# Optimization experiments

Hardware: AMD Instinct MI355X
Metric: run time of the kernel (lower is better)

Reference implementation:

```python
import jax, jax.numpy as jnp
import numpy as np

N = 50000      # nodes
E = 800000     # edges (avg degree 16)
D = 256        # d_model
H = 8          # heads
C = D // H     # per-head channels = 32
DE = 64        # edge feature dim
NEG_SLOPE = 0.2
EPS = 1e-5


def setup_inputs() -> dict:
    key = jax.random.key(0)
    ks = jax.random.split(key, 12)
    s = 0.05
    return {
        "x": jax.random.normal(ks[0], (N, D), jnp.float32),
        "edge_attr": jax.random.normal(ks[1], (E, DE), jnp.float32),
        "edge_index": jax.random.randint(ks[2], (2, E), 0, N, dtype=jnp.int32),
        # GATv2Conv params (torch Linear layout: [out, in])
        "W_l": jax.random.normal(ks[3], (H * C, D), jnp.float32) * s,   # lin_l (source)
        "b_l": jnp.zeros((H * C,), jnp.float32),
        "W_r": jax.random.normal(ks[4], (H * C, D), jnp.float32) * s,   # lin_r (target)
        "b_r": jnp.zeros((H * C,), jnp.float32),
        "W_e": jax.random.normal(ks[5], (H * C, DE), jnp.float32) * s,  # lin_edge (no bias)
        "att": jax.random.normal(ks[6], (H, C), jnp.float32) * s,       # attention vector a
        "W_res": jax.random.normal(ks[7], (H * C, D), jnp.float32) * s, # residual Linear (no bias)
        "bias": jnp.zeros((H * C,), jnp.float32),                        # conv output bias
        "gamma": jnp.ones((D,), jnp.float32),                            # LayerNorm weight
        "beta": jnp.zeros((D,), jnp.float32),                            # LayerNorm bias
    }


def reference(x, edge_attr, W_l, b_l, W_r, b_r, W_e, att, W_res, bias, gamma, beta, edge_index):
    src = edge_index[0]  # j (messages flow source -> target)
    dst = edge_index[1]  # i

    xl = (x @ W_l.T + b_l).reshape(N, H, C)   # source transform
    xr = (x @ W_r.T + b_r).reshape(N, H, C)   # target transform
    ee = (edge_attr @ W_e.T).reshape(E, H, C)  # edge embedding

    # GATv2 attention logits per edge/head
    g = jax.nn.leaky_relu(xl[src] + xr[dst] + ee, NEG_SLOPE)  # [E, H, C]
    alpha = jnp.einsum("ehc,hc->eh", g, att)                   # [E, H]

    # segment softmax over incoming edges of each target node
    amax = jax.ops.segment_max(alpha, dst, num_segments=N)     # [N, H] (-inf for empty)
    ealpha = jnp.exp(alpha - amax[dst])
    denom = jax.ops.segment_sum(ealpha, dst, num_segments=N)   # [N, H]
    alpha = ealpha / jnp.where(denom > 0, denom, 1.0)[dst]

    # weighted message aggregation (scatter-add)
    msg = xl[src] * alpha[:, :, None]                          # [E, H, C]
    out = jax.ops.segment_sum(msg, dst, num_segments=N)        # [N, H, C]

    out = out.reshape(N, H * C) + x @ W_res.T + bias           # concat heads + residual + bias

    # LayerNorm over last dim
    mu = out.mean(-1, keepdims=True)
    var = ((out - mu) ** 2).mean(-1, keepdims=True)
    return (out - mu) * jax.lax.rsqrt(var + EPS) * gamma + beta
```

## Files before the change

kernel.cpp:

```cpp
#include <hip/hip_runtime.h>

#define N_NODES 50000
#define N_EDGES 800000
#define D_MODEL 256
#define H_HEADS 8
#define C_CH 32
#define DE_DIM 64
#define NEG_SLOPE 0.2f
#define LN_EPS 1e-5f
#define TILES (N_EDGES / 64)

typedef float  f32x4  __attribute__((ext_vector_type(4)));
typedef short  bf16x8 __attribute__((ext_vector_type(8)));

static __device__ __forceinline__ unsigned short f2bf(float f) {
    unsigned int u = __float_as_uint(f);
    u += 0x7fffu + ((u >> 16) & 1u);
    return (unsigned short)(u >> 16);
}
static __device__ __forceinline__ float bf2f(unsigned short s) {
    return __uint_as_float(((unsigned int)s) << 16);
}
static __device__ __forceinline__ bf16x8 load_cvt8(const float* __restrict__ p) {
    float4 a = *(const float4*)p;
    float4 b = *(const float4*)(p + 4);
    bf16x8 r;
    r[0] = (short)f2bf(a.x); r[1] = (short)f2bf(a.y);
    r[2] = (short)f2bf(a.z); r[3] = (short)f2bf(a.w);
    r[4] = (short)f2bf(b.x); r[5] = (short)f2bf(b.y);
    r[6] = (short)f2bf(b.z); r[7] = (short)f2bf(b.w);
    return r;
}

__global__ __launch_bounds__(256) void cvt_bf16_kernel(const float* __restrict__ in,
                                                       unsigned short* __restrict__ out,
                                                       int n8) {
    int g = blockIdx.x * 256 + threadIdx.x;
    if (g < n8) {
        bf16x8 v = load_cvt8(in + (size_t)g * 8);
        *(bf16x8*)(out + (size_t)g * 8) = v;
    }
}

__global__ __launch_bounds__(256) void node_gemm(const unsigned short* __restrict__ xbf,
                                                 const unsigned short* __restrict__ Wbf,
                                                 const float* __restrict__ bl,
                                                 const float* __restrict__ br,
                                                 unsigned short* __restrict__ xl,
                                                 unsigned short* __restrict__ xr,
                                                 float* __restrict__ res) {
    int tid = threadIdx.x;
    int lane = tid & 63, wv = tid >> 6;
    int quad = lane >> 4, l15 = lane & 15;
    int rowTile = blockIdx.x * 64;
    int which = blockIdx.y;
    const unsigned short* W = Wbf + (size_t)which * 65536;
    int colBase = wv * 64;

    f32x4 acc[4][4];
#pragma unroll
    for (int r = 0; r < 4; r++)
#pragma unroll
        for (int c = 0; c < 4; c++) acc[r][c] = (f32x4){0.f, 0.f, 0.f, 0.f};

#pragma unroll 1
    for (int k8 = 0; k8 < 8; ++k8) {
        int kb = k8 * 32 + quad * 8;
        bf16x8 af[4], bfr[4];
#pragma unroll
        for (int r = 0; r < 4; r++) {
            int row = rowTile + r * 16 + l15;
            if (row > N_NODES - 1) row = N_NODES - 1;
            af[r] = *(const bf16x8*)(xbf + (size_t)row * D_MODEL + kb);
        }
#pragma unroll
        for (int c = 0; c < 4; c++) {
            int col = colBase + c * 16 + l15;
            bfr[c] = *(const bf16x8*)(W + (size_t)col * D_MODEL + kb);
        }
#pragma unroll
        for (int r = 0; r < 4; r++)
#pragma unroll
            for (int c = 0; c < 4; c++)
                acc[r][c] = __builtin_amdgcn_mfma_f32_16x16x32_bf16(af[r], bfr[c], acc[r][c], 0, 0, 0);
    }

    float bv[4];
#pragma unroll
    for (int c = 0; c < 4; c++) {
        int col = colBase + c * 16 + l15;
        bv[c] = (which == 0) ? bl[col] : (which == 1 ? br[col] : 0.f);
    }
#pragma unroll
    for (int r = 0; r < 4; r++) {
#pragma unroll
        for (int g = 0; g < 4; g++) {
            int row = rowTile + r * 16 + quad * 4 + g;
            if (row < N_NODES) {
#pragma unroll
                for (int c = 0; c < 4; c++) {
                    int col = colBase + c * 16 + l15;
                    float v = acc[r][c][g] + bv[c];
                    size_t idx = (size_t)row * D_MODEL + col;
                    if (which == 0)      xl[idx] = f2bf(v);
                    else if (which == 1) xr[idx] = f2bf(v);
                    else                 res[idx] = v;
                }
            }
        }
    }
}

__global__ __launch_bounds__(256) void edge_logits(const float* __restrict__ edge_attr,
                                                   const float* __restrict__ We,
                                                   const float* __restrict__ att,
                                                   const int* __restrict__ srcIdx,
                                                   const int* __restrict__ dstIdx,
                                                   const int* __restrict__ posOf,
                                                   const unsigned short* __restrict__ xl,
                                                   const unsigned short* __restrict__ xr,
                                                   float* __restrict__ alphaP) {
    __shared__ short weS[2048 * 8];

    int tid = threadIdx.x;
    int lane = tid & 63, wv = tid >> 6;
    int quad = lane >> 4, l15 = lane & 15;

    for (int g = tid; g < 2048; g += 256) {
        int c = g >> 7, kq = (g >> 6) & 1, ln = g & 63;
        int o = c * 16 + (ln & 15);
        int k = kq * 32 + (ln >> 4) * 8;
        bf16x8 v = load_cvt8(We + o * DE_DIM + k);
        *(bf16x8*)&weS[g * 8] = v;
    }
    __syncthreads();

    for (int tile = blockIdx.x; tile < TILES; tile += gridDim.x) {
        int e = tile * 64 + wv * 16 + l15;
        int srcv = srcIdx[e];
        int dstv = dstIdx[e];
        int posv = posOf[e];

        bf16x8 a0 = load_cvt8(edge_attr + (size_t)e * DE_DIM + quad * 8);
        bf16x8 a1 = load_cvt8(edge_attr + (size_t)e * DE_DIM + 32 + quad * 8);

        const unsigned short* xlr = xl + (size_t)srcv * D_MODEL + quad * 4;
        const unsigned short* xrr = xr + (size_t)dstv * D_MODEL + quad * 4;

        float pa[8];
#pragma unroll
        for (int h = 0; h < 8; h++) pa[h] = 0.f;

#pragma unroll
        for (int c = 0; c < 16; c++) {
            bf16x8 b0 = *(bf16x8*)&weS[((c * 2 + 0) * 64 + lane) * 8];
            bf16x8 b1 = *(bf16x8*)&weS[((c * 2 + 1) * 64 + lane) * 8];
            f32x4 ee = (f32x4){0.f, 0.f, 0.f, 0.f};
            ee = __builtin_amdgcn_mfma_f32_16x16x32_bf16(b0, a0, ee, 0, 0, 0);
            ee = __builtin_amdgcn_mfma_f32_16x16x32_bf16(b1, a1, ee, 0, 0, 0);
            ushort4 x4 = *(const ushort4*)(xlr + c * 16);
            ushort4 r4 = *(const ushort4*)(xrr + c * 16);
            f32x4 av = *(const f32x4*)(att + c * 16 + quad * 4);
            float s = 0.f;
            float t0 = ee[0] + bf2f(x4.x) + bf2f(r4.x);
            float t1 = ee[1] + bf2f(x4.y) + bf2f(r4.y);
            float t2 = ee[2] + bf2f(x4.z) + bf2f(r4.z);
            float t3 = ee[3] + bf2f(x4.w) + bf2f(r4.w);
            t0 = (t0 > 0.f) ? t0 : NEG_SLOPE * t0;
            t1 = (t1 > 0.f) ? t1 : NEG_SLOPE * t1;
            t2 = (t2 > 0.f) ? t2 : NEG_SLOPE * t2;
            t3 = (t3 > 0.f) ? t3 : NEG_SLOPE * t3;
            s = fmaf(t0, av[0], s);
            s = fmaf(t1, av[1], s);
            s = fmaf(t2, av[2], s);
            s = fmaf(t3, av[3], s);
            pa[c >> 1] += s;
        }
#pragma unroll
        for (int h = 0; h < 8; h++) {
            float v = pa[h];
            v += __shfl_xor(v, 16);
            v += __shfl_xor(v, 32);
            pa[h] = v;
        }
        if (quad == 0) {
            float4 w0 = make_float4(pa[0], pa[1], pa[2], pa[3]);
            *(float4*)(alphaP + (size_t)posv * 8) = w0;
        } else if (quad == 1) {
            float4 w1 = make_float4(pa[4], pa[5], pa[6], pa[7]);
            *(float4*)(alphaP + (size_t)posv * 8 + 4) = w1;
        }
    }
}

__global__ __launch_bounds__(256) void hist_kernel(const int* __restrict__ dstIdx,
                                                   int* __restrict__ cnt) {
    int e = blockIdx.x * 256 + threadIdx.x;
    if (e < N_EDGES) atomicAdd(&cnt[dstIdx[e]], 1);
}

__global__ __launch_bounds__(1024) void scan_kernel(const int* __restrict__ cnt,
                                                    int* __restrict__ off,
                                                    int* __restrict__ woff) {
    const int CHUNK = 49;
    int tid = threadIdx.x;
    int base = tid * CHUNK;
    int local[CHUNK];
    int sum = 0;
#pragma unroll
    for (int j = 0; j < CHUNK; ++j) {
        int idx = base + j;
        int v = (idx < N_NODES) ? cnt[idx] : 0;
        local[j] = sum;
        sum += v;
    }
    int lane = tid & 63, wv = tid >> 6;
    int s = sum;
#pragma unroll
    for (int ofs = 1; ofs < 64; ofs <<= 1) {
        int t2 = __shfl_up(s, ofs);
        if (lane >= ofs) s += t2;
    }
    __shared__ int wsum[16];
    __shared__ int woffS[16];
    if (lane == 63) wsum[wv] = s;
    __syncthreads();
    if (tid == 0) {
        int a = 0;
#pragma unroll
        for (int i = 0; i < 16; ++i) { woffS[i] = a; a += wsum[i]; }
    }
    __syncthreads();
    int excl = woffS[wv] + (s - sum);
#pragma unroll
    for (int j = 0; j < CHUNK; ++j) {
        int idx = base + j;
        if (idx < N_NODES) {
            int v = excl + local[j];
            off[idx] = v;
            woff[idx] = v;
        }
    }
    if (tid == 0) off[N_NODES] = N_EDGES;
}

__global__ __launch_bounds__(256) void scatter_kernel(const int* __restrict__ srcIdx,
                                                      const int* __restrict__ dstIdx,
                                                      int* __restrict__ woff,
                                                      int* __restrict__ posOf,
                                                      int* __restrict__ srcP) {
    int e = blockIdx.x * 256 + threadIdx.x;
    if (e < N_EDGES) {
        int pos = atomicAdd(&woff[dstIdx[e]], 1);
        posOf[e] = pos;
        srcP[pos] = srcIdx[e];
    }
}

__global__ __launch_bounds__(256) void aggregate_ln(const int* __restrict__ off,
                                                    const int* __restrict__ srcP,
                                                    const float* __restrict__ alphaP,
                                                    const unsigned short* __restrict__ xl,
                                                    const float* __restrict__ res,
                                                    const float* __restrict__ biasc,
                                                    const float* __restrict__ gamma,
                                                    const float* __restrict__ beta,
                                                    float* __restrict__ out) {
    int wv = threadIdx.x >> 6, lane = threadIdx.x & 63;
    int i = blockIdx.x * 4 + wv;
    int beg = off[i], end = off[i + 1];
    int h = lane >> 3;

    float acc0 = 0.f, acc1 = 0.f, acc2 = 0.f, acc3 = 0.f, s = 0.f;

    int p = beg;
    int src_n = 0; float a_n = 0.f;
    if (p < end) {
        src_n = srcP[p];
        a_n   = alphaP[(size_t)p * 8 + h];
    }
    while (p < end) {
        int src = src_n; float a = a_n;
        int pn = p + 1;
        if (pn < end) {
            src_n = srcP[pn];
            a_n   = alphaP[(size_t)pn * 8 + h];
        }
        ushort4 v = *(const ushort4*)(xl + (size_t)src * D_MODEL + lane * 4);
        float w = __expf(a);
        s += w;
        acc0 = fmaf(w, bf2f(v.x), acc0);
        acc1 = fmaf(w, bf2f(v.y), acc1);
        acc2 = fmaf(w, bf2f(v.z), acc2);
        acc3 = fmaf(w, bf2f(v.w), acc3);
        p = pn;
    }

    float rs = (end > beg) ? (1.f / s) : 0.f;
    float4 r4 = *(const float4*)(res + (size_t)i * D_MODEL + lane * 4);
    float4 b4 = *(const float4*)(biasc + lane * 4);
    float v0 = acc0 * rs + r4.x + b4.x;
    float v1 = acc1 * rs + r4.y + b4.y;
    float v2 = acc2 * rs + r4.z + b4.z;
    float v3 = acc3 * rs + r4.w + b4.w;

    float sum = v0 + v1 + v2 + v3;
    float sq  = v0 * v0 + v1 * v1 + v2 * v2 + v3 * v3;
#pragma unroll
    for (int msk = 32; msk >= 1; msk >>= 1) {
        sum += __shfl_xor(sum, msk);
        sq  += __shfl_xor(sq, msk);
    }
    float mu  = sum * (1.f / 256.f);
    float var = sq * (1.f / 256.f) - mu * mu;
    var = fmaxf(var, 0.f);
    float inv = rsqrtf(var + LN_EPS);

    float4 g4 = *(const float4*)(gamma + lane * 4);
    float4 be4 = *(const float4*)(beta + lane * 4);
    float4 o4;
    o4.x = (v0 - mu) * inv * g4.x + be4.x;
    o4.y = (v1 - mu) * inv * g4.y + be4.y;
    o4.z = (v2 - mu) * inv * g4.z + be4.z;
    o4.w = (v3 - mu) * inv * g4.w + be4.w;
    *(float4*)(out + (size_t)i * D_MODEL + lane * 4) = o4;
}

extern "C" void kernel_launch(void* const* d_in, const int* in_sizes, int n_in,
                              void* d_out, int out_size, void* d_ws, size_t ws_size,
                              hipStream_t stream) {
    const float* x         = (const float*)d_in[0];
    const float* edge_attr = (const float*)d_in[1];
    const int*   edge_index= (const int*)d_in[2];
    const float* Wl        = (const float*)d_in[3];
    const float* bl        = (const float*)d_in[4];
    const float* Wr        = (const float*)d_in[5];
    const float* br        = (const float*)d_in[6];
    const float* We        = (const float*)d_in[7];
    const float* att       = (const float*)d_in[8];
    const float* Wres      = (const float*)d_in[9];
    const float* biasc     = (const float*)d_in[10];
    const float* gamma     = (const float*)d_in[11];
    const float* beta      = (const float*)d_in[12];
    const int* srcIdx = edge_index;
    const int* dstIdx = edge_index + N_EDGES;
    float* out = (float*)d_out;

    char* ws = (char*)d_ws;
    unsigned short* xl  = (unsigned short*)ws;
    unsigned short* xr  = xl + (size_t)N_NODES * D_MODEL;
    unsigned short* xbf = xr + (size_t)N_NODES * D_MODEL;
    unsigned short* Wbf = xbf + (size_t)N_NODES * D_MODEL;
    float* res    = (float*)(Wbf + 3 * 65536);
    float* alphaP = res + (size_t)N_NODES * D_MODEL;
    int* cnt   = (int*)(alphaP + (size_t)N_EDGES * 8);
    int* off   = cnt + N_NODES;
    int* woff  = off + (N_NODES + 1);
    int* posOf = woff + N_NODES;
    int* srcP  = posOf + N_EDGES;
    (void)ws_size; (void)n_in; (void)in_sizes; (void)out_size;

    hipMemsetAsync(cnt, 0, N_NODES * sizeof(int), stream);

    cvt_bf16_kernel<<<(N_NODES * D_MODEL / 8 + 255) / 256, 256, 0, stream>>>(x, xbf, N_NODES * D_MODEL / 8);
    cvt_bf16_kernel<<<32, 256, 0, stream>>>(Wl,   Wbf,             65536 / 8);
    cvt_bf16_kernel<<<32, 256, 0, stream>>>(Wr,   Wbf + 65536,     65536 / 8);
    cvt_bf16_kernel<<<32, 256, 0, stream>>>(Wres, Wbf + 2 * 65536, 65536 / 8);

    dim3 g1((N_NODES + 63) / 64, 3);
    node_gemm<<<g1, 256, 0, stream>>>(xbf, Wbf, bl, br, xl, xr, res);

    hist_kernel<<<(N_EDGES + 255) / 256, 256, 0, stream>>>(dstIdx, cnt);
    scan_kernel<<<1, 1024, 0, stream>>>(cnt, off, woff);
    scatter_kernel<<<(N_EDGES + 255) / 256, 256, 0, stream>>>(srcIdx, dstIdx, woff, posOf, srcP);

    edge_logits<<<1280, 256, 0, stream>>>(edge_attr, We, att, srcIdx, dstIdx, posOf, xl, xr, alphaP);

    aggregate_ln<<<N_NODES / 4, 256, 0, stream>>>(off, srcP, alphaP, xl, res,
                                                  biasc, gamma, beta, out);
}
```

Before: 974.5 us.

## Process edges in destination-sorted order with transposed MFMA output mapping in edge_logits

The scatter kernel now records, for each sorted position, the destination and original edge id. edge_logits walks edges in CSR order, so alpha writes are contiguous and xr rows of the same destination are reused across neighbouring edges. The MFMA operands are swapped so each lane owns one column across four edges, which makes xl/xr gathers scalar bf16 loads coalesced along columns. It also needs a 16-lane shuffle reduction, adds a gather of edge_attr through eP, and changes the grid from 1280 to 1024 blocks.

```diff
diff --git a/kernel.cpp b/kernel.cpp
--- a/kernel.cpp
+++ b/kernel.cpp
@@ -114,9 +114,9 @@
 __global__ __launch_bounds__(256) void edge_logits(const float* __restrict__ edge_attr,
                                                    const float* __restrict__ We,
                                                    const float* __restrict__ att,
-                                                   const int* __restrict__ srcIdx,
-                                                   const int* __restrict__ dstIdx,
-                                                   const int* __restrict__ posOf,
+                                                   const int* __restrict__ srcP,
+                                                   const int* __restrict__ dstP,
+                                                   const int* __restrict__ eP,
                                                    const unsigned short* __restrict__ xl,
                                                    const unsigned short* __restrict__ xr,
                                                    float* __restrict__ alphaP) {
@@ -135,60 +135,67 @@
     }
     __syncthreads();
 
+    float attv[16];
+#pragma unroll
+    for (int c = 0; c < 16; c++) attv[c] = att[c * 16 + l15];
+
     for (int tile = blockIdx.x; tile < TILES; tile += gridDim.x) {
-        int e = tile * 64 + wv * 16 + l15;
-        int srcv = srcIdx[e];
-        int dstv = dstIdx[e];
-        int posv = posOf[e];
-
-        bf16x8 a0 = load_cvt8(edge_attr + (size_t)e * DE_DIM + quad * 8);
-        bf16x8 a1 = load_cvt8(edge_attr + (size_t)e * DE_DIM + 32 + quad * 8);
-
-        const unsigned short* xlr = xl + (size_t)srcv * D_MODEL + quad * 4;
-        const unsigned short* xrr = xr + (size_t)dstv * D_MODEL + quad * 4;
-
-        float pa[8];
-#pragma unroll
-        for (int h = 0; h < 8; h++) pa[h] = 0.f;
+        int p0 = tile * 64 + wv * 16;
+
+        int ef = eP[p0 + l15];
+        bf16x8 a0 = load_cvt8(edge_attr + (size_t)ef * DE_DIM + quad * 8);
+        bf16x8 a1 = load_cvt8(edge_attr + (size_t)ef * DE_DIM + 32 + quad * 8);
+
+        int srcv[4], dstv[4];
+#pragma unroll
+        for (int r = 0; r < 4; r++) {
+            int p = p0 + quad * 4 + r;
+            srcv[r] = srcP[p];
+            dstv[r] = dstP[p];
+        }
+
+        float pa[4][8];
+#pragma unroll
+        for (int r = 0; r < 4; r++)
+#pragma unroll
+            for (int h = 0; h < 8; h++) pa[r][h] = 0.f;
 
 #pragma unroll
         for (int c = 0; c < 16; c++) {
             bf16x8 b0 = *(bf16x8*)&weS[((c * 2 + 0) * 64 + lane) * 8];
             bf16x8 b1 = *(bf16x8*)&weS[((c * 2 + 1) * 64 + lane) * 8];
             f32x4 ee = (f32x4){0.f, 0.f, 0.f, 0.f};
-            ee = __builtin_amdgcn_mfma_f32_16x16x32_bf16(b0, a0, ee, 0, 0, 0);
-            ee = __builtin_amdgcn_mfma_f32_16x16x32_bf16(b1, a1, ee, 0, 0, 0);
-            ushort4 x4 = *(const ushort4*)(xlr + c * 16);
-            ushort4 r4 = *(const ushort4*)(xrr + c * 16);
-            f32x4 av = *(const f32x4*)(att + c * 16 + quad * 4);
-            float s = 0.f;
-            float t0 = ee[0] + bf2f(x4.x) + bf2f(r4.x);
-            float t1 = ee[1] + bf2f(x4.y) + bf2f(r4.y);
-            float t2 = ee[2] + bf2f(x4.z) + bf2f(r4.z);
-            float t3 = ee[3] + bf2f(x4.w) + bf2f(r4.w);
-            t0 = (t0 > 0.f) ? t0 : NEG_SLOPE * t0;
-            t1 = (t1 > 0.f) ? t1 : NEG_SLOPE * t1;
-            t2 = (t2 > 0.f) ? t2 : NEG_SLOPE * t2;
-            t3 = (t3 > 0.f) ? t3 : NEG_SLOPE * t3;
-            s = fmaf(t0, av[0], s);
-            s = fmaf(t1, av[1], s);
-            s = fmaf(t2, av[2], s);
-            s = fmaf(t3, av[3], s);
-            pa[c >> 1] += s;
-        }
-#pragma unroll
-        for (int h = 0; h < 8; h++) {
-            float v = pa[h];
-            v += __shfl_xor(v, 16);
-            v += __shfl_xor(v, 32);
-            pa[h] = v;
-        }
-        if (quad == 0) {
-            float4 w0 = make_float4(pa[0], pa[1], pa[2], pa[3]);
-            *(float4*)(alphaP + (size_t)posv * 8) = w0;
-        } else if (quad == 1) {
-            float4 w1 = make_float4(pa[4], pa[5], pa[6], pa[7]);
-            *(float4*)(alphaP + (size_t)posv * 8 + 4) = w1;
+            ee = __builtin_amdgcn_mfma_f32_16x16x32_bf16(a0, b0, ee, 0, 0, 0);
+            ee = __builtin_amdgcn_mfma_f32_16x16x32_bf16(a1, b1, ee, 0, 0, 0);
+            int col = c * 16 + l15;
+            float attvc = attv[c];
+#pragma unroll
+            for (int r = 0; r < 4; r++) {
+                float xlv = bf2f(xl[(size_t)srcv[r] * D_MODEL + col]);
+                float xrv = bf2f(xr[(size_t)dstv[r] * D_MODEL + col]);
+                float t = ee[r] + xlv + xrv;
+                t = (t > 0.f) ? t : NEG_SLOPE * t;
+                pa[r][c >> 1] += t * attvc;
+            }
+        }
+#pragma unroll
+        for (int r = 0; r < 4; r++)
+#pragma unroll
+            for (int h = 0; h < 8; h++) {
+                float v = pa[r][h];
+                v += __shfl_xor(v, 1);
+                v += __shfl_xor(v, 2);
+                v += __shfl_xor(v, 4);
+                v += __shfl_xor(v, 8);
+                pa[r][h] = v;
+            }
+        if (l15 == 0) {
+#pragma unroll
+            for (int r = 0; r < 4; r++) {
+                size_t pos = (size_t)(p0 + quad * 4 + r);
+                *(float4*)(alphaP + pos * 8)     = make_float4(pa[r][0], pa[r][1], pa[r][2], pa[r][3]);
+                *(float4*)(alphaP + pos * 8 + 4) = make_float4(pa[r][4], pa[r][5], pa[r][6], pa[r][7]);
+            }
         }
     }
 }
@@ -247,13 +254,16 @@
 __global__ __launch_bounds__(256) void scatter_kernel(const int* __restrict__ srcIdx,
                                                       const int* __restrict__ dstIdx,
                                                       int* __restrict__ woff,
-                                                      int* __restrict__ posOf,
-                                                      int* __restrict__ srcP) {
+                                                      int* __restrict__ srcP,
+                                                      int* __restrict__ dstP,
+                                                      int* __restrict__ eP) {
     int e = blockIdx.x * 256 + threadIdx.x;
     if (e < N_EDGES) {
-        int pos = atomicAdd(&woff[dstIdx[e]], 1);
-        posOf[e] = pos;
+        int d = dstIdx[e];
+        int pos = atomicAdd(&woff[d], 1);
         srcP[pos] = srcIdx[e];
+        dstP[pos] = d;
+        eP[pos]   = e;
     }
 }
 
@@ -356,8 +366,9 @@
     int* cnt   = (int*)(alphaP + (size_t)N_EDGES * 8);
     int* off   = cnt + N_NODES;
     int* woff  = off + (N_NODES + 1);
-    int* posOf = woff + N_NODES;
-    int* srcP  = posOf + N_EDGES;
+    int* srcP  = woff + N_NODES;
+    int* dstP  = srcP + N_EDGES;
+    int* eP    = dstP + N_EDGES;
     (void)ws_size; (void)n_in; (void)in_sizes; (void)out_size;
 
     hipMemsetAsync(cnt, 0, N_NODES * sizeof(int), stream);
@@ -372,9 +383,9 @@
 
     hist_kernel<<<(N_EDGES + 255) / 256, 256, 0, stream>>>(dstIdx, cnt);
     scan_kernel<<<1, 1024, 0, stream>>>(cnt, off, woff);
-    scatter_kernel<<<(N_EDGES + 255) / 256, 256, 0, stream>>>(srcIdx, dstIdx, woff, posOf, srcP);
-
-    edge_logits<<<1280, 256, 0, stream>>>(edge_attr, We, att, srcIdx, dstIdx, posOf, xl, xr, alphaP);
+    scatter_kernel<<<(N_EDGES + 255) / 256, 256, 0, stream>>>(srcIdx, dstIdx, woff, srcP, dstP, eP);
+
+    edge_logits<<<1024, 256, 0, stream>>>(edge_attr, We, att, srcP, dstP, eP, xl, xr, alphaP);
 
     aggregate_ln<<<N_NODES / 4, 256, 0, stream>>>(off, srcP, alphaP, xl, res,
                                                   biasc, gamma, beta, out);
```

New measurement: 1.035 ms. +6.2%, slower.
